# Optimization experiments

Hardware: AMD Instinct MI355X
Metric: run time of the kernel (lower is better)

The kernel has to match this reference:

```python
import jax, jax.numpy as jnp
import numpy as np

D_EMBED = 1024
N_HEAD = 16
LEN_TRIM = 1024
LN_EPS = 1e-5


def setup_inputs() -> dict:
    key = jax.random.key(0)
    ks = jax.random.split(key, 8)
    B = 2
    h_q = jax.random.normal(ks[0], (B, LEN_TRIM, D_EMBED), jnp.float32)
    h_kv1 = jax.random.normal(ks[1], (B, LEN_TRIM, D_EMBED), jnp.float32)
    h_kv2 = jax.random.normal(ks[2], (B, 2 * LEN_TRIM, D_EMBED), jnp.float32)
    mask = jax.random.uniform(ks[3], (B, LEN_TRIM, 1), jnp.float32)
    in_proj_w = jax.random.normal(ks[4], (3 * D_EMBED, D_EMBED), jnp.float32) * 0.02
    in_proj_b = jnp.zeros((3 * D_EMBED,), jnp.float32)
    out_w = jax.random.normal(ks[5], (D_EMBED, D_EMBED), jnp.float32) * 0.02
    out_b = jnp.zeros((D_EMBED,), jnp.float32)
    ln_g = jnp.ones((D_EMBED,), jnp.float32)
    ln_b = jnp.zeros((D_EMBED,), jnp.float32)
    return dict(h_q=h_q, h_kv1=h_kv1, h_kv2=h_kv2, mask=mask,
                in_proj_w=in_proj_w, in_proj_b=in_proj_b,
                out_w=out_w, out_b=out_b, ln_g=ln_g, ln_b=ln_b)


def _layernorm(x, g, b):
    mu = jnp.mean(x, axis=-1, keepdims=True)
    var = jnp.mean(jnp.square(x - mu), axis=-1, keepdims=True)
    return (x - mu) * jax.lax.rsqrt(var + LN_EPS) * g + b


def reference(h_q, h_kv1, h_kv2, mask, in_proj_w, in_proj_b, out_w, out_b, ln_g, ln_b):
    B, L, D = h_q.shape
    H = N_HEAD
    dh = D // H
    h_kv = jnp.concatenate((h_kv1, h_kv2), axis=1)  # (B, 3L, D)
    S = h_kv.shape[1]
    Wq, Wk, Wv = jnp.split(in_proj_w, 3, axis=0)
    bq, bk, bv = jnp.split(in_proj_b, 3, axis=0)
    q = (h_q @ Wq.T + bq).reshape(B, L, H, dh).transpose(0, 2, 1, 3)   # (B,H,L,dh)
    k = (h_kv @ Wk.T + bk).reshape(B, S, H, dh).transpose(0, 2, 1, 3)  # (B,H,S,dh)
    v = (h_kv @ Wv.T + bv).reshape(B, S, H, dh).transpose(0, 2, 1, 3)
    scores = jnp.einsum('bhld,bhsd->bhls', q, k) / jnp.sqrt(jnp.float32(dh))
    block = jnp.triu(jnp.ones((L, L), bool), k=1)
    mask_causal = jnp.concatenate((block, block, block), axis=-1)  # (L, S)
    scores = jnp.where(mask_causal, -jnp.inf, scores)
    attn = jax.nn.softmax(scores, axis=-1)
    ctx = jnp.einsum('bhls,bhsd->bhld', attn, v).transpose(0, 2, 1, 3).reshape(B, L, D)
    attn_out = ctx @ out_w.T + out_b
    return _layernorm(h_q + attn_out, ln_g, ln_b) * mask
```

## Files before the change

### kernel.cpp

```cpp
#include <hip/hip_runtime.h>
#include <stdint.h>

typedef unsigned short u16;
typedef unsigned int u32;
typedef __bf16 bf16x8 __attribute__((ext_vector_type(8)));
typedef float floatx4 __attribute__((ext_vector_type(4)));
typedef u16 u16x8 __attribute__((ext_vector_type(8)));
typedef u16 u16x4 __attribute__((ext_vector_type(4)));

__device__ __forceinline__ u16 f2bf(float f) {
    __bf16 h = (__bf16)f;
    return __builtin_bit_cast(u16, h);
}

__device__ __forceinline__ void gll16(const u16* g, u16* l) {
    typedef __attribute__((address_space(1))) u32 gu32;
    typedef __attribute__((address_space(3))) u32 lu32;
    __builtin_amdgcn_global_load_lds((gu32*)g, (lu32*)l, 16, 0, 0);
}

__global__ __launch_bounds__(256) void cvt_all(const float* __restrict__ hq,
                                               const float* __restrict__ kv1,
                                               const float* __restrict__ kv2,
                                               const float* __restrict__ win,
                                               u16* __restrict__ a_q,
                                               u16* __restrict__ a_kv,
                                               u16* __restrict__ wb) {
    const int NQ = 262144, NKV = 786432, NW = 393216;
    int i = blockIdx.x * 256 + threadIdx.x;
    const int stride = gridDim.x * 256;
    for (; i < NQ + NKV + NW; i += stride) {
        const float* src; u16* dst;
        if (i < NQ) {
            src = hq + (long long)i * 8; dst = a_q + (long long)i * 8;
        } else if (i < NQ + NKV) {
            int c = i - NQ;
            int row = c >> 7;
            int col = (c & 127) * 8;
            int b = row >= 3072, r = row - b * 3072;
            src = (r < 1024) ? kv1 + ((long long)(b * 1024 + r)) * 1024 + col
                             : kv2 + ((long long)(b * 2048 + (r - 1024))) * 1024 + col;
            dst = a_kv + (long long)row * 1024 + col;
        } else {
            int c = i - (NQ + NKV);
            src = win + (long long)c * 8; dst = wb + (long long)c * 8;
        }
        floatx4 x = *(const floatx4*)src;
        floatx4 y = *(const floatx4*)(src + 4);
        u16x8 o;
        #pragma unroll
        for (int j = 0; j < 4; j++) { o[j] = f2bf(x[j]); o[4 + j] = f2bf(y[j]); }
        *(u16x8*)dst = o;
    }
}

__global__ __launch_bounds__(256) void cvt_bf16(const float* __restrict__ in,
                                                u16* __restrict__ out, int n8) {
    int i = blockIdx.x * 256 + threadIdx.x;
    const int stride = gridDim.x * 256;
    for (; i < n8; i += stride) {
        floatx4 a = *(const floatx4*)(in + (long long)i * 8);
        floatx4 b = *(const floatx4*)(in + (long long)i * 8 + 4);
        u16x8 o;
        #pragma unroll
        for (int j = 0; j < 4; j++) { o[j] = f2bf(a[j]); o[4 + j] = f2bf(b[j]); }
        *(u16x8*)(out + (long long)i * 8) = o;
    }
}

__global__ __launch_bounds__(256) void gemm_proj(const u16* __restrict__ aq,
                                                 const u16* __restrict__ akv,
                                                 const u16* __restrict__ wb,
                                                 const float* __restrict__ bias,
                                                 u16* __restrict__ Qo,
                                                 u16* __restrict__ Ko,
                                                 u16* __restrict__ VTg) {
    __shared__ u16 lds[2][2][8192];
    const int tid = threadIdx.x;
    const int wave = tid >> 6, lane = tid & 63;
    const int lane16 = lane & 15, quad = lane >> 4;
    const int bid = blockIdx.x;
    const int g = (bid & 7) * 112 + (bid >> 3);
    const bool qblk = g < 128;
    int my, nx;
    if (qblk) { my = g >> 3; nx = g & 7; }
    else { int gg = g - 128; my = gg >> 4; nx = gg & 15; }
    const int rowBase = my * 128;
    const int colBase = nx * 128;
    const int wrow = (qblk ? 0 : 1024) + colBase;
    const int wm = (wave >> 1) * 64, wn = (wave & 1) * 64;

    floatx4 acc[4][4];
    #pragma unroll
    for (int am = 0; am < 4; am++)
        #pragma unroll
        for (int bn = 0; bn < 4; bn++) acc[am][bn] = floatx4{0.f, 0.f, 0.f, 0.f};

    const int srow8 = tid >> 3;
    const int scol = ((tid & 7) ^ (srow8 & 7)) * 8;
    const u16* aS = (qblk ? aq : akv) + (long long)(rowBase + srow8) * 1024 + scol;
    const u16* bS = wb + (long long)(wrow + srow8) * 1024 + scol;
    u16* lbase = &lds[0][0][0];
    const int ldst = wave * 512;

    const int cko0 = ((quad ^ (lane16 & 7)) * 8);
    const int cko1 = (((4 + quad) ^ (lane16 & 7)) * 8);

    {
        u16* dA = lbase; u16* dB = lbase + 8192;
        #pragma unroll
        for (int j = 0; j < 4; j++) {
            gll16(aS + j * 32768, dA + j * 2048 + ldst);
            gll16(bS + j * 32768, dB + j * 2048 + ldst);
        }
    }
    __syncthreads();

    int buf = 0;
    for (int t = 0; t < 16; t++) {
        if (t < 15) {
            const int k0 = (t + 1) * 64;
            u16* dA = lbase + (buf ^ 1) * 16384;
            u16* dB = dA + 8192;
            #pragma unroll
            for (int j = 0; j < 4; j++) {
                gll16(aS + j * 32768 + k0, dA + j * 2048 + ldst);
                gll16(bS + j * 32768 + k0, dB + j * 2048 + ldst);
            }
        }
        const u16* Ab = lbase + buf * 16384;
        const u16* Bb = Ab + 8192;
        u16x8 a0[4], a1[4], b0[4], b1[4];
        #pragma unroll
        for (int i = 0; i < 4; i++) {
            a0[i] = *(const u16x8*)&Ab[(wm + i * 16 + lane16) * 64 + cko0];
            a1[i] = *(const u16x8*)&Ab[(wm + i * 16 + lane16) * 64 + cko1];
            b0[i] = *(const u16x8*)&Bb[(wn + i * 16 + lane16) * 64 + cko0];
            b1[i] = *(const u16x8*)&Bb[(wn + i * 16 + lane16) * 64 + cko1];
        }
        #pragma unroll
        for (int am = 0; am < 4; am++)
            #pragma unroll
            for (int bn = 0; bn < 4; bn++)
                acc[am][bn] = __builtin_amdgcn_mfma_f32_16x16x32_bf16(
                    __builtin_bit_cast(bf16x8, a0[am]),
                    __builtin_bit_cast(bf16x8, b0[bn]), acc[am][bn], 0, 0, 0);
        #pragma unroll
        for (int am = 0; am < 4; am++)
            #pragma unroll
            for (int bn = 0; bn < 4; bn++)
                acc[am][bn] = __builtin_amdgcn_mfma_f32_16x16x32_bf16(
                    __builtin_bit_cast(bf16x8, a1[am]),
                    __builtin_bit_cast(bf16x8, b1[bn]), acc[am][bn], 0, 0, 0);
        __syncthreads();
        buf ^= 1;
    }

    const float* bcol = bias + (qblk ? 0 : 1024) + colBase;
    if (qblk || nx < 8) {
        u16* Cb = qblk ? Qo : Ko;
        #pragma unroll
        for (int am = 0; am < 4; am++)
            #pragma unroll
            for (int bn = 0; bn < 4; bn++)
                #pragma unroll
                for (int r = 0; r < 4; r++) {
                    int row = rowBase + wm + am * 16 + quad * 4 + r;
                    int col = wn + bn * 16 + lane16;
                    float v = acc[am][bn][r] + bcol[col];
                    if (qblk) v *= 0.1803368801f;
                    Cb[(long long)row * 1024 + colBase + col] = f2bf(v);
                }
    } else {
        const int b_ = rowBase >= 3072;
        const int keyBase = rowBase - b_ * 3072 + wm;
        #pragma unroll
        for (int am = 0; am < 4; am++)
            #pragma unroll
            for (int bn = 0; bn < 4; bn++) {
                int col = wn + bn * 16 + lane16;
                int d = colBase - 1024 + col;
                int key0 = keyBase + am * 16 + quad * 4;
                u16x4 pk;
                #pragma unroll
                for (int r = 0; r < 4; r++) pk[r] = f2bf(acc[am][bn][r] + bcol[col]);
                *(u16x4*)&VTg[((long long)(b_ * 1024 + d)) * 3072 + key0] = pk;
            }
    }
}

__global__ __launch_bounds__(256) void gemm_out(const u16* __restrict__ ctx,
                                                const u16* __restrict__ wob,
                                                const float* __restrict__ bias,
                                                float* __restrict__ ao0,
                                                float* __restrict__ ao1) {
    __shared__ u16 lds[2][2][8192];
    const int tid = threadIdx.x;
    const int wave = tid >> 6, lane = tid & 63;
    const int lane16 = lane & 15, quad = lane >> 4;
    const int bid = blockIdx.x;
    const int g = (bid & 7) * 32 + (bid >> 3);
    const int my = g >> 4;
    const int nx = (g & 15) >> 1;
    const int kh = g & 1;
    const int rowBase = my * 128, colBase = nx * 128, kbase = kh * 512;
    const int wm = (wave >> 1) * 64, wn = (wave & 1) * 64;

    floatx4 acc[4][4];
    #pragma unroll
    for (int am = 0; am < 4; am++)
        #pragma unroll
        for (int bn = 0; bn < 4; bn++) acc[am][bn] = floatx4{0.f, 0.f, 0.f, 0.f};

    const int srow8 = tid >> 3;
    const int scol = ((tid & 7) ^ (srow8 & 7)) * 8;
    const u16* aS = ctx + (long long)(rowBase + srow8) * 1024 + kbase + scol;
    const u16* bS = wob + (long long)(colBase + srow8) * 1024 + kbase + scol;
    u16* lbase = &lds[0][0][0];
    const int ldst = wave * 512;
    const int cko0 = ((quad ^ (lane16 & 7)) * 8);
    const int cko1 = (((4 + quad) ^ (lane16 & 7)) * 8);

    {
        u16* dA = lbase; u16* dB = lbase + 8192;
        #pragma unroll
        for (int j = 0; j < 4; j++) {
            gll16(aS + j * 32768, dA + j * 2048 + ldst);
            gll16(bS + j * 32768, dB + j * 2048 + ldst);
        }
    }
    __syncthreads();

    int buf = 0;
    for (int t = 0; t < 8; t++) {
        if (t < 7) {
            const int k0 = (t + 1) * 64;
            u16* dA = lbase + (buf ^ 1) * 16384;
            u16* dB = dA + 8192;
            #pragma unroll
            for (int j = 0; j < 4; j++) {
                gll16(aS + j * 32768 + k0, dA + j * 2048 + ldst);
                gll16(bS + j * 32768 + k0, dB + j * 2048 + ldst);
            }
        }
        const u16* Ab = lbase + buf * 16384;
        const u16* Bb = Ab + 8192;
        u16x8 a0[4], a1[4], b0[4], b1[4];
        #pragma unroll
        for (int i = 0; i < 4; i++) {
            a0[i] = *(const u16x8*)&Ab[(wm + i * 16 + lane16) * 64 + cko0];
            a1[i] = *(const u16x8*)&Ab[(wm + i * 16 + lane16) * 64 + cko1];
            b0[i] = *(const u16x8*)&Bb[(wn + i * 16 + lane16) * 64 + cko0];
            b1[i] = *(const u16x8*)&Bb[(wn + i * 16 + lane16) * 64 + cko1];
        }
        #pragma unroll
        for (int am = 0; am < 4; am++)
            #pragma unroll
            for (int bn = 0; bn < 4; bn++)
                acc[am][bn] = __builtin_amdgcn_mfma_f32_16x16x32_bf16(
                    __builtin_bit_cast(bf16x8, a0[am]),
                    __builtin_bit_cast(bf16x8, b0[bn]), acc[am][bn], 0, 0, 0);
        #pragma unroll
        for (int am = 0; am < 4; am++)
            #pragma unroll
            for (int bn = 0; bn < 4; bn++)
                acc[am][bn] = __builtin_amdgcn_mfma_f32_16x16x32_bf16(
                    __builtin_bit_cast(bf16x8, a1[am]),
                    __builtin_bit_cast(bf16x8, b1[bn]), acc[am][bn], 0, 0, 0);
        __syncthreads();
        buf ^= 1;
    }

    float* Co = kh ? ao1 : ao0;
    #pragma unroll
    for (int am = 0; am < 4; am++)
        #pragma unroll
        for (int bn = 0; bn < 4; bn++)
            #pragma unroll
            for (int r = 0; r < 4; r++) {
                int row = rowBase + wm + am * 16 + quad * 4 + r;
                int col = colBase + wn + bn * 16 + lane16;
                float v = acc[am][bn][r] + (kh == 0 ? bias[col] : 0.f);
                Co[(long long)row * 1024 + col] = v;
            }
}

#define ATTN_TILE(DIAG_, HAVENEXT_)                                           \
{                                                                             \
    const int cur = t & 1;                                                    \
    if (HAVENEXT_) {                                                          \
        const long long ko = (long long)(t + 1) * 65536;                      \
        const long long vo = (long long)(t + 1) * 64;                         \
        _Pragma("unroll")                                                     \
        for (int j = 0; j < 2; j++) {                                         \
            gll16(kS + ko + j * 32768, &Kt[cur ^ 1][j * 2048 + ldst]);        \
            gll16(vS + vo + (long long)j * 32 * 3072, &Vt[cur ^ 1][j * 2048 + ldst]); \
        }                                                                     \
        asm volatile("s_waitcnt vmcnt(4)" ::: "memory");   \
    } else {                                                                  \
        asm volatile("s_waitcnt vmcnt(0)" ::: "memory");                      \
    }                                                                         \
    __builtin_amdgcn_sched_barrier(0);                                        \
    floatx4 sacc[4];                                                          \
    _Pragma("unroll")                                                         \
    for (int mi = 0; mi < 4; mi++) sacc[mi] = floatx4{0.f, 0.f, 0.f, 0.f};    \
    __builtin_amdgcn_s_setprio(1);                                            \
    _Pragma("unroll")                                                         \
    for (int mi = 0; mi < 4; mi++) {                                          \
        u16x8 kf = *(const u16x8*)&Kt[cur][(mi * 16 + lane16) * 64 + slot0];  \
        sacc[mi] = __builtin_amdgcn_mfma_f32_16x16x32_bf16(                   \
            __builtin_bit_cast(bf16x8, kf), qf[0], sacc[mi], 0, 0, 0);        \
    }                                                                         \
    _Pragma("unroll")                                                         \
    for (int mi = 0; mi < 4; mi++) {                                          \
        u16x8 kf = *(const u16x8*)&Kt[cur][(mi * 16 + lane16) * 64 + slot1];  \
        sacc[mi] = __builtin_amdgcn_mfma_f32_16x16x32_bf16(                   \
            __builtin_bit_cast(bf16x8, kf), qf[1], sacc[mi], 0, 0, 0);        \
    }                                                                         \
    __builtin_amdgcn_s_setprio(0);                                            \
    if (DIAG_) {                                \
        _Pragma("unroll")                                                     \
        for (int mi = 0; mi < 4; mi++)                                        \
            _Pragma("unroll")                                                 \
            for (int r = 0; r < 4; r++)                                       \
                if ((mi * 16 + quad * 4 + r) > qloc) sacc[mi][r] = -1e30f;    \
    }                                                                         \
    float tmax = fmaxf(sacc[0][0], sacc[0][1]);                               \
    tmax = fmaxf(tmax, fmaxf(sacc[0][2], sacc[0][3]));                        \
    _Pragma("unroll")                                                         \
    for (int mi = 1; mi < 4; mi++) {                                          \
        tmax = fmaxf(tmax, fmaxf(sacc[mi][0], sacc[mi][1]));                  \
        tmax = fmaxf(tmax, fmaxf(sacc[mi][2], sacc[mi][3]));                  \
    }                                                                         \
    if (!__all(tmax <= m_i + 8.0f)) {           \
        float tr = fmaxf(tmax, __shfl_xor(tmax, 16));                         \
        tr = fmaxf(tr, __shfl_xor(tr, 32));                                   \
        float m_new = fmaxf(m_i, tr);                                         \
        float alpha = exp2f(m_i - m_new);                                     \
        _Pragma("unroll")                                                     \
        for (int mi = 0; mi < 4; mi++)                                        \
            _Pragma("unroll")                                                 \
            for (int r = 0; r < 4; r++) o_acc[mi][r] *= alpha;                \
        l_acc[0] *= alpha;                         \
        m_i = m_new;                                                          \
    }                                                                         \
    _Pragma("unroll")                                                         \
    for (int mi = 0; mi < 4; mi++) {                                          \
        u16x4 pk;                                                             \
        _Pragma("unroll")                                                     \
        for (int r = 0; r < 4; r++) pk[r] = f2bf(exp2f(sacc[mi][r] - m_i));   \
        *(u16x4*)&Ps[wave][lane16 * 64 +                                      \
            (((mi * 2 + (quad >> 1)) ^ (lane16 & 7)) << 3) + (quad & 1) * 4] = pk; \
    }                                                                         \
    __builtin_amdgcn_wave_barrier();                                          \
    __builtin_amdgcn_s_setprio(1);                                            \
    _Pragma("unroll")                                                         \
    for (int c = 0; c < 2; c++) {                                             \
        bf16x8 pf = __builtin_bit_cast(bf16x8, *(const u16x8*)&Ps[wave][      \
            lane16 * 64 + (((c * 4 + quad) ^ (lane16 & 7)) << 3)]);           \
        const int slot = c ? slot1 : slot0;                                   \
        _Pragma("unroll")                                                     \
        for (int mi = 0; mi < 4; mi++) {                                      \
            bf16x8 vf = __builtin_bit_cast(bf16x8,                            \
                *(const u16x8*)&Vt[cur][(mi * 16 + lane16) * 64 + slot]);     \
            o_acc[mi] = __builtin_amdgcn_mfma_f32_16x16x32_bf16(vf, pf, o_acc[mi], 0, 0, 0); \
        }                                                                     \
        l_acc = __builtin_amdgcn_mfma_f32_16x16x32_bf16(onesf, pf, l_acc, 0, 0, 0); \
    }                                                                         \
    __builtin_amdgcn_s_setprio(0);                                            \
    if (HAVENEXT_) {                            \
        asm volatile("s_waitcnt lgkmcnt(0)" ::: "memory");                    \
        __builtin_amdgcn_s_barrier();                                         \
        __builtin_amdgcn_sched_barrier(0);                                    \
    }                                                                         \
}

__global__ __launch_bounds__(256) void attn_seg(const u16* __restrict__ Q,
                                                const u16* __restrict__ Kb,
                                                const u16* __restrict__ VTg,
                                                float* __restrict__ pO_lo,
                                                float* __restrict__ pO_hi,
                                                float* __restrict__ pml) {
    __shared__ u16 Kt[2][4096];
    __shared__ u16 Vt[2][4096];
    __shared__ u16 Ps[4][1024];
    const int tid = threadIdx.x;
    const int wave = tid >> 6, lane = tid & 63;
    const int lane16 = lane & 15, quad = lane >> 4;
    const int bid = blockIdx.x;
    const int qrank = bid / 96;
    const int r_    = bid - qrank * 96;
    const int qt  = 15 - qrank;
    const int b   = r_ / 48;
    const int r2  = r_ - b * 48;
    const int seg = r2 >> 4;
    const int h   = r2 & 15;
    const int l0 = qt * 64;
    const int wq = wave * 16;
    const int qloc = wq + lane16;

    bf16x8 qf[2];
    {
        const u16* qrow = Q + ((long long)(b * 1024 + l0 + wq + lane16)) * 1024 + h * 64;
        qf[0] = __builtin_bit_cast(bf16x8, *(const u16x8*)(qrow + quad * 8));
        qf[1] = __builtin_bit_cast(bf16x8, *(const u16x8*)(qrow + 32 + quad * 8));
    }
    u16x8 onesu;
    #pragma unroll
    for (int j = 0; j < 8; j++) onesu[j] = 0x3F80;
    const bf16x8 onesf = __builtin_bit_cast(bf16x8, onesu);

    const int srow = tid >> 3;
    const int csw8 = ((tid & 7) ^ (srow & 7)) * 8;
    const long long bh = ((long long)b * 3072) * 1024 + h * 64;
    const u16* kS = Kb + bh + ((long long)(seg * 1024)) * 1024
                    + (long long)srow * 1024 + csw8;
    const u16* vS = VTg + ((long long)(b * 1024 + h * 64 + srow)) * 3072
                    + seg * 1024 + csw8;
    const int ldst = wave * 512;

    {
        #pragma unroll
        for (int j = 0; j < 2; j++) {
            gll16(kS + j * 32768, &Kt[0][j * 2048 + ldst]);
            gll16(vS + (long long)j * 32 * 3072, &Vt[0][j * 2048 + ldst]);
        }
    }
    __syncthreads();

    const int slot0 = ((quad ^ (lane16 & 7)) * 8);
    const int slot1 = (((4 + quad) ^ (lane16 & 7)) * 8);

    float m_i = -1e30f;
    floatx4 o_acc[4];
    floatx4 l_acc = floatx4{0.f, 0.f, 0.f, 0.f};
    #pragma unroll
    for (int mi = 0; mi < 4; mi++) o_acc[mi] = floatx4{0.f, 0.f, 0.f, 0.f};

    for (int t = 0; t < qt; t++) ATTN_TILE(false, true)
    { int t = qt; ATTN_TILE(true, false) }

    const float l_i = l_acc[0];

    const int p = ((b * 16 + h) * 16 + qt) * 3 + seg;
    float* op = (p < 512) ? (pO_lo + (long long)p * 4096)
                          : (pO_hi + (long long)(p - 512) * 4096);
    if (quad == 0) {
        pml[(long long)p * 128 + (wq + lane16) * 2]     = m_i;
        pml[(long long)p * 128 + (wq + lane16) * 2 + 1] = l_i;
    }
    float* orow = op + (long long)(wq + lane16) * 64;
    #pragma unroll
    for (int mi = 0; mi < 4; mi++)
        *(floatx4*)(orow + mi * 16 + quad * 4) = o_acc[mi];
}

__global__ __launch_bounds__(256) void attn_combine(const float* __restrict__ pO_lo,
                                                    const float* __restrict__ pO_hi,
                                                    const float* __restrict__ pml,
                                                    u16* __restrict__ Ctx) {
    const int g = blockIdx.x;
    const int qt = g & 15;
    const int h  = (g >> 4) & 15;
    const int b  = g >> 8;
    const int t  = threadIdx.x;
    const int q  = t >> 2;
    const int d0 = (t & 3) * 16;
    const int p0 = g * 3;

    float m[3], l[3];
    #pragma unroll
    for (int s = 0; s < 3; s++) {
        m[s] = pml[(long long)(p0 + s) * 128 + q * 2];
        l[s] = pml[(long long)(p0 + s) * 128 + q * 2 + 1];
    }
    float M = fmaxf(m[0], fmaxf(m[1], m[2]));
    float w[3];
    #pragma unroll
    for (int s = 0; s < 3; s++) w[s] = exp2f(m[s] - M);
    float L = w[0] * l[0] + w[1] * l[1] + w[2] * l[2];
    float invL = 1.0f / L;

    const float* O[3];
    #pragma unroll
    for (int s = 0; s < 3; s++) {
        int pp = p0 + s;
        O[s] = ((pp < 512) ? (pO_lo + (long long)pp * 4096)
                           : (pO_hi + (long long)(pp - 512) * 4096))
               + (long long)q * 64 + d0;
    }

    long long crow = ((long long)(b * 1024 + qt * 64 + q)) * 1024 + h * 64 + d0;
    #pragma unroll
    for (int i = 0; i < 16; i += 4) {
        floatx4 a  = *(const floatx4*)(O[0] + i);
        floatx4 bb = *(const floatx4*)(O[1] + i);
        floatx4 cc = *(const floatx4*)(O[2] + i);
        #pragma unroll
        for (int j = 0; j < 4; j++)
            Ctx[crow + i + j] = f2bf((w[0] * a[j] + w[1] * bb[j] + w[2] * cc[j]) * invL);
    }
}

__global__ __launch_bounds__(256) void ln_kernel(const float* __restrict__ AO0,
                                                 const float* __restrict__ AO1,
                                                 const float* __restrict__ HQ,
                                                 const float* __restrict__ g,
                                                 const float* __restrict__ bb,
                                                 const float* __restrict__ mask,
                                                 float* __restrict__ Out) {
    const int row = blockIdx.x;
    const int t = threadIdx.x;
    const int base = row * 1024 + t * 4;
    floatx4 a0 = *(const floatx4*)&AO0[base];
    floatx4 a1 = *(const floatx4*)&AO1[base];
    floatx4 hq = *(const floatx4*)&HQ[base];
    float x[4];
    #pragma unroll
    for (int i = 0; i < 4; i++) x[i] = a0[i] + a1[i] + hq[i];
    float s = x[0] + x[1] + x[2] + x[3];
    float ss = x[0]*x[0] + x[1]*x[1] + x[2]*x[2] + x[3]*x[3];
    #pragma unroll
    for (int off = 32; off >= 1; off >>= 1) { s += __shfl_xor(s, off); ss += __shfl_xor(ss, off); }
    __shared__ float smem[8];
    int wave = t >> 6, lane = t & 63;
    if (lane == 0) { smem[wave] = s; smem[4 + wave] = ss; }
    __syncthreads();
    s  = smem[0] + smem[1] + smem[2] + smem[3];
    ss = smem[4] + smem[5] + smem[6] + smem[7];
    float mu  = s * (1.f / 1024.f);
    float var = ss * (1.f / 1024.f) - mu * mu;
    float rs  = rsqrtf(var + 1e-5f);
    float mv  = mask[row];
    floatx4 g4 = *(const floatx4*)&g[t * 4];
    floatx4 b4 = *(const floatx4*)&bb[t * 4];
    floatx4 y4;
    #pragma unroll
    for (int i = 0; i < 4; i++) y4[i] = ((x[i] - mu) * rs * g4[i] + b4[i]) * mv;
    *(floatx4*)&Out[base] = y4;
}

extern "C" void kernel_launch(void* const* d_in, const int* in_sizes, int n_in,
                              void* d_out, int out_size, void* d_ws, size_t ws_size,
                              hipStream_t stream) {
    (void)in_sizes; (void)n_in; (void)out_size; (void)ws_size;
    const float* h_q   = (const float*)d_in[0];
    const float* h_kv1 = (const float*)d_in[1];
    const float* h_kv2 = (const float*)d_in[2];
    const float* maskp = (const float*)d_in[3];
    const float* win   = (const float*)d_in[4];
    const float* binp  = (const float*)d_in[5];
    const float* wout  = (const float*)d_in[6];
    const float* bout  = (const float*)d_in[7];
    const float* ln_g  = (const float*)d_in[8];
    const float* ln_b  = (const float*)d_in[9];
    float* outp = (float*)d_out;

    char* ws = (char*)d_ws;
    const size_t MB = 1024 * 1024;
    u16*   q_b   = (u16*)(ws);
    u16*   k_b   = (u16*)(ws + 4 * MB);
    u16*   vT    = (u16*)(ws + 16 * MB);
    u16*   ctx_b = q_b;
    u16*   a_q   = (u16*)(ws + 28 * MB);
    u16*   a_kv  = (u16*)(ws + 32 * MB);
    u16*   wb    = (u16*)d_out;
    float* pO_lo = (float*)d_out;
    float* pO_hi = (float*)(ws + 28 * MB);
    u16*   wob   = (u16*)(ws + 28 * MB);
    float* pml   = (float*)(ws + 44 * MB);
    float* ao0   = (float*)(ws + 4 * MB);
    float* ao1   = (float*)(ws + 12 * MB);

    cvt_all<<<2048, 256, 0, stream>>>(h_q, h_kv1, h_kv2, win, a_q, a_kv, wb);
    gemm_proj<<<896, 256, 0, stream>>>(a_q, a_kv, wb, binp, q_b, k_b, vT);
    attn_seg<<<1536, 256, 0, stream>>>(q_b, k_b, vT, pO_lo, pO_hi, pml);
    attn_combine<<<512, 256, 0, stream>>>(pO_lo, pO_hi, pml, ctx_b);
    cvt_bf16<<<512, 256, 0, stream>>>(wout, wob, 131072);
    gemm_out<<<256, 256, 0, stream>>>(ctx_b, wob, bout, ao0, ao1);
    ln_kernel<<<2048, 256, 0, stream>>>(ao0, ao1, h_q, ln_g, ln_b, maskp, outp);
}
```

Before: 209.9 us.

## Halve GEMM K-tile to 32 with panel-major LDS layout and explicit waitcnt pipelining

Both projection and output GEMMs now stage K=32 per step instead of 64, storing A/B tiles in a panel-major LDS layout (8-element k-panels by 128 rows) rather than the XOR-swizzled row layout. This halves LDS usage per block, which allows higher occupancy. The prefetch wait becomes an explicit vmcnt wait plus a raw s_barrier instead of __syncthreads, and MFMA issue is raised to high priority. The cost is twice as many loop iterations and barriers per tile. The attention tile macro also gains an extra s_barrier after its vmcnt wait, which is presumably needed so all waves' async LDS loads are visible before use.

```diff
diff --git a/kernel.cpp b/kernel.cpp
--- a/kernel.cpp
+++ b/kernel.cpp
@@ -75,7 +75,7 @@
                                                  u16* __restrict__ Qo,
                                                  u16* __restrict__ Ko,
                                                  u16* __restrict__ VTg) {
-    __shared__ u16 lds[2][2][8192];
+    __shared__ u16 lds[2][2][4096];
     const int tid = threadIdx.x;
     const int wave = tid >> 6, lane = tid & 63;
     const int lane16 = lane & 15, quad = lane >> 4;
@@ -96,63 +96,57 @@
         #pragma unroll
         for (int bn = 0; bn < 4; bn++) acc[am][bn] = floatx4{0.f, 0.f, 0.f, 0.f};
 
-    const int srow8 = tid >> 3;
-    const int scol = ((tid & 7) ^ (srow8 & 7)) * 8;
-    const u16* aS = (qblk ? aq : akv) + (long long)(rowBase + srow8) * 1024 + scol;
-    const u16* bS = wb + (long long)(wrow + srow8) * 1024 + scol;
+    const int srow = tid & 127;
+    const int pan8 = (tid >> 7) * 8;
+    const u16* aS = (qblk ? aq : akv) + (long long)(rowBase + srow) * 1024 + pan8;
+    const u16* bS = wb + (long long)(wrow + srow) * 1024 + pan8;
     u16* lbase = &lds[0][0][0];
     const int ldst = wave * 512;
 
-    const int cko0 = ((quad ^ (lane16 & 7)) * 8);
-    const int cko1 = (((4 + quad) ^ (lane16 & 7)) * 8);
-
     {
-        u16* dA = lbase; u16* dB = lbase + 8192;
-        #pragma unroll
-        for (int j = 0; j < 4; j++) {
-            gll16(aS + j * 32768, dA + j * 2048 + ldst);
-            gll16(bS + j * 32768, dB + j * 2048 + ldst);
+        gll16(aS,      lbase        + ldst);
+        gll16(aS + 16, lbase + 2048 + ldst);
+        gll16(bS,      lbase + 4096 + ldst);
+        gll16(bS + 16, lbase + 6144 + ldst);
+    }
+    __syncthreads();
+
+    const int fpan = quad * 1024;
+    int buf = 0;
+    for (int t = 0; t < 32; t++) {
+        if (t < 31) {
+            const int k0 = (t + 1) * 32;
+            u16* d = lbase + (buf ^ 1) * 8192;
+            gll16(aS + k0,      d        + ldst);
+            gll16(aS + k0 + 16, d + 2048 + ldst);
+            gll16(bS + k0,      d + 4096 + ldst);
+            gll16(bS + k0 + 16, d + 6144 + ldst);
+            asm volatile("s_waitcnt vmcnt(4)" ::: "memory");
+        } else {
+            asm volatile("s_waitcnt vmcnt(0)" ::: "memory");
         }
-    }
-    __syncthreads();
-
-    int buf = 0;
-    for (int t = 0; t < 16; t++) {
-        if (t < 15) {
-            const int k0 = (t + 1) * 64;
-            u16* dA = lbase + (buf ^ 1) * 16384;
-            u16* dB = dA + 8192;
-            #pragma unroll
-            for (int j = 0; j < 4; j++) {
-                gll16(aS + j * 32768 + k0, dA + j * 2048 + ldst);
-                gll16(bS + j * 32768 + k0, dB + j * 2048 + ldst);
-            }
+        __builtin_amdgcn_s_barrier();
+        __builtin_amdgcn_sched_barrier(0);
+        const u16* Ab = lbase + buf * 8192;
+        const u16* Bb = Ab + 4096;
+        u16x8 af[4], bf[4];
+        #pragma unroll
+        for (int i = 0; i < 4; i++) {
+            af[i] = *(const u16x8*)&Ab[fpan + (wm + i * 16 + lane16) * 8];
+            bf[i] = *(const u16x8*)&Bb[fpan + (wn + i * 16 + lane16) * 8];
         }
-        const u16* Ab = lbase + buf * 16384;
-        const u16* Bb = Ab + 8192;
-        u16x8 a0[4], a1[4], b0[4], b1[4];
-        #pragma unroll
-        for (int i = 0; i < 4; i++) {
-            a0[i] = *(const u16x8*)&Ab[(wm + i * 16 + lane16) * 64 + cko0];
-            a1[i] = *(const u16x8*)&Ab[(wm + i * 16 + lane16) * 64 + cko1];
-            b0[i] = *(const u16x8*)&Bb[(wn + i * 16 + lane16) * 64 + cko0];
-            b1[i] = *(const u16x8*)&Bb[(wn + i * 16 + lane16) * 64 + cko1];
-        }
+        __builtin_amdgcn_s_setprio(1);
         #pragma unroll
         for (int am = 0; am < 4; am++)
             #pragma unroll
             for (int bn = 0; bn < 4; bn++)
                 acc[am][bn] = __builtin_amdgcn_mfma_f32_16x16x32_bf16(
-                    __builtin_bit_cast(bf16x8, a0[am]),
-                    __builtin_bit_cast(bf16x8, b0[bn]), acc[am][bn], 0, 0, 0);
-        #pragma unroll
-        for (int am = 0; am < 4; am++)
-            #pragma unroll
-            for (int bn = 0; bn < 4; bn++)
-                acc[am][bn] = __builtin_amdgcn_mfma_f32_16x16x32_bf16(
-                    __builtin_bit_cast(bf16x8, a1[am]),
-                    __builtin_bit_cast(bf16x8, b1[bn]), acc[am][bn], 0, 0, 0);
-        __syncthreads();
+                    __builtin_bit_cast(bf16x8, af[am]),
+                    __builtin_bit_cast(bf16x8, bf[bn]), acc[am][bn], 0, 0, 0);
+        __builtin_amdgcn_s_setprio(0);
+        asm volatile("s_waitcnt lgkmcnt(0)" ::: "memory");
+        __builtin_amdgcn_s_barrier();
+        __builtin_amdgcn_sched_barrier(0);
         buf ^= 1;
     }
 
@@ -194,7 +188,7 @@
                                                 const float* __restrict__ bias,
                                                 float* __restrict__ ao0,
                                                 float* __restrict__ ao1) {
-    __shared__ u16 lds[2][2][8192];
+    __shared__ u16 lds[2][2][4096];
     const int tid = threadIdx.x;
     const int wave = tid >> 6, lane = tid & 63;
     const int lane16 = lane & 15, quad = lane >> 4;
@@ -212,62 +206,57 @@
         #pragma unroll
         for (int bn = 0; bn < 4; bn++) acc[am][bn] = floatx4{0.f, 0.f, 0.f, 0.f};
 
-    const int srow8 = tid >> 3;
-    const int scol = ((tid & 7) ^ (srow8 & 7)) * 8;
-    const u16* aS = ctx + (long long)(rowBase + srow8) * 1024 + kbase + scol;
-    const u16* bS = wob + (long long)(colBase + srow8) * 1024 + kbase + scol;
+    const int srow = tid & 127;
+    const int pan8 = (tid >> 7) * 8;
+    const u16* aS = ctx + (long long)(rowBase + srow) * 1024 + kbase + pan8;
+    const u16* bS = wob + (long long)(colBase + srow) * 1024 + kbase + pan8;
     u16* lbase = &lds[0][0][0];
     const int ldst = wave * 512;
-    const int cko0 = ((quad ^ (lane16 & 7)) * 8);
-    const int cko1 = (((4 + quad) ^ (lane16 & 7)) * 8);
 
     {
-        u16* dA = lbase; u16* dB = lbase + 8192;
-        #pragma unroll
-        for (int j = 0; j < 4; j++) {
-            gll16(aS + j * 32768, dA + j * 2048 + ldst);
-            gll16(bS + j * 32768, dB + j * 2048 + ldst);
+        gll16(aS,      lbase        + ldst);
+        gll16(aS + 16, lbase + 2048 + ldst);
+        gll16(bS,      lbase + 4096 + ldst);
+        gll16(bS + 16, lbase + 6144 + ldst);
+    }
+    __syncthreads();
+
+    const int fpan = quad * 1024;
+    int buf = 0;
+    for (int t = 0; t < 16; t++) {
+        if (t < 15) {
+            const int k0 = (t + 1) * 32;
+            u16* d = lbase + (buf ^ 1) * 8192;
+            gll16(aS + k0,      d        + ldst);
+            gll16(aS + k0 + 16, d + 2048 + ldst);
+            gll16(bS + k0,      d + 4096 + ldst);
+            gll16(bS + k0 + 16, d + 6144 + ldst);
+            asm volatile("s_waitcnt vmcnt(4)" ::: "memory");
+        } else {
+            asm volatile("s_waitcnt vmcnt(0)" ::: "memory");
         }
-    }
-    __syncthreads();
-
-    int buf = 0;
-    for (int t = 0; t < 8; t++) {
-        if (t < 7) {
-            const int k0 = (t + 1) * 64;
-            u16* dA = lbase + (buf ^ 1) * 16384;
-            u16* dB = dA + 8192;
-            #pragma unroll
-            for (int j = 0; j < 4; j++) {
-                gll16(aS + j * 32768 + k0, dA + j * 2048 + ldst);
-                gll16(bS + j * 32768 + k0, dB + j * 2048 + ldst);
-            }
+        __builtin_amdgcn_s_barrier();
+        __builtin_amdgcn_sched_barrier(0);
+        const u16* Ab = lbase + buf * 8192;
+        const u16* Bb = Ab + 4096;
+        u16x8 af[4], bf[4];
+        #pragma unroll
+        for (int i = 0; i < 4; i++) {
+            af[i] = *(const u16x8*)&Ab[fpan + (wm + i * 16 + lane16) * 8];
+            bf[i] = *(const u16x8*)&Bb[fpan + (wn + i * 16 + lane16) * 8];
         }
-        const u16* Ab = lbase + buf * 16384;
-        const u16* Bb = Ab + 8192;
-        u16x8 a0[4], a1[4], b0[4], b1[4];
-        #pragma unroll
-        for (int i = 0; i < 4; i++) {
-            a0[i] = *(const u16x8*)&Ab[(wm + i * 16 + lane16) * 64 + cko0];
-            a1[i] = *(const u16x8*)&Ab[(wm + i * 16 + lane16) * 64 + cko1];
-            b0[i] = *(const u16x8*)&Bb[(wn + i * 16 + lane16) * 64 + cko0];
-            b1[i] = *(const u16x8*)&Bb[(wn + i * 16 + lane16) * 64 + cko1];
-        }
+        __builtin_amdgcn_s_setprio(1);
         #pragma unroll
         for (int am = 0; am < 4; am++)
             #pragma unroll
             for (int bn = 0; bn < 4; bn++)
                 acc[am][bn] = __builtin_amdgcn_mfma_f32_16x16x32_bf16(
-                    __builtin_bit_cast(bf16x8, a0[am]),
-                    __builtin_bit_cast(bf16x8, b0[bn]), acc[am][bn], 0, 0, 0);
-        #pragma unroll
-        for (int am = 0; am < 4; am++)
-            #pragma unroll
-            for (int bn = 0; bn < 4; bn++)
-                acc[am][bn] = __builtin_amdgcn_mfma_f32_16x16x32_bf16(
-                    __builtin_bit_cast(bf16x8, a1[am]),
-                    __builtin_bit_cast(bf16x8, b1[bn]), acc[am][bn], 0, 0, 0);
-        __syncthreads();
+                    __builtin_bit_cast(bf16x8, af[am]),
+                    __builtin_bit_cast(bf16x8, bf[bn]), acc[am][bn], 0, 0, 0);
+        __builtin_amdgcn_s_setprio(0);
+        asm volatile("s_waitcnt lgkmcnt(0)" ::: "memory");
+        __builtin_amdgcn_s_barrier();
+        __builtin_amdgcn_sched_barrier(0);
         buf ^= 1;
     }
 
@@ -300,6 +289,7 @@
     } else {                                                                  \
         asm volatile("s_waitcnt vmcnt(0)" ::: "memory");                      \
     }                                                                         \
+    __builtin_amdgcn_s_barrier();                  \
     __builtin_amdgcn_sched_barrier(0);                                        \
     floatx4 sacc[4];                                                          \
     _Pragma("unroll")                                                         \
```

Result: slower. 246.4 us (+17.4%).
